# Performance work log

Measured on AMD Instinct MI355X. Metric: run time of the kernel, lower is better.

## Reference

```python
import jax, jax.numpy as jnp
import numpy as np
import math

L, V, D, H, T, B = 12, 50257, 1024, 16, 1024, 1
HD = D // H
EPS = 1e-5


def layernorm(x, g, b):
    m = jnp.mean(x, axis=-1, keepdims=True)
    v = jnp.var(x, axis=-1, keepdims=True)
    return (x - m) * jax.lax.rsqrt(v + EPS) * g + b


def gelu_tanh(x):
    return 0.5 * x * (1.0 + jnp.tanh(math.sqrt(2.0 / math.pi) * (x + 0.044715 * x ** 3)))


def setup_inputs() -> dict:
    key = jax.random.key(0)
    ks = jax.random.split(key, 16)
    s = 0.02
    inp = {
        "x": jax.random.randint(ks[0], (B, T), 0, V),
        "attention_mask": jnp.ones((B, T), jnp.float32),
        "tok_emb": jax.random.normal(ks[1], (V, D), jnp.float32) * s,
        "pos_emb": jax.random.normal(ks[2], (T, D), jnp.float32) * s,
        "ln1_g": jnp.ones((L, D), jnp.float32),
        "ln1_b": jnp.zeros((L, D), jnp.float32),
        "qkv_w": jax.random.normal(ks[3], (L, D, 3 * D), jnp.float32) * s,
        "qkv_b": jnp.zeros((L, 3 * D), jnp.float32),
        "out_w": jax.random.normal(ks[4], (L, D, D), jnp.float32) * s,
        "out_b": jnp.zeros((L, D), jnp.float32),
        "ln2_g": jnp.ones((L, D), jnp.float32),
        "ln2_b": jnp.zeros((L, D), jnp.float32),
        "fc1_w": jax.random.normal(ks[5], (L, D, 4 * D), jnp.float32) * s,
        "fc1_b": jnp.zeros((L, 4 * D), jnp.float32),
        "fc2_w": jax.random.normal(ks[6], (L, 4 * D, D), jnp.float32) * s,
        "fc2_b": jnp.zeros((L, D), jnp.float32),
        "lnf_g": jnp.ones((D,), jnp.float32),
        "lnf_b": jnp.zeros((D,), jnp.float32),
        "lm_w": jax.random.normal(ks[7], (V, D), jnp.float32) * s,
    }
    return inp


def reference(x, attention_mask, tok_emb, pos_emb, ln1_g, ln1_b, qkv_w, qkv_b,
              out_w, out_b, ln2_g, ln2_b, fc1_w, fc1_b, fc2_w, fc2_b,
              lnf_g, lnf_b, lm_w):
    Bx, Tx = x.shape
    h = tok_emb[x] + pos_emb[:Tx]  # (B,T,D)
    causal = jnp.tril(jnp.ones((Tx, Tx), bool))  # (T,T)
    amask_add = (1.0 - attention_mask)[:, None, None, :] * jnp.finfo(h.dtype).min
    scale = 1.0 / math.sqrt(HD)

    def block(h, p):
        l1g, l1b, qw, qb, ow, ob, l2g, l2b, f1w, f1b, f2w, f2b = p
        xn = layernorm(h, l1g, l1b)
        qkv = xn @ qw + qb  # (B,T,3D)
        q, k, v = jnp.split(qkv, 3, axis=-1)
        q = q.reshape(Bx, Tx, H, HD).transpose(0, 2, 1, 3)  # (B,H,T,hd)
        k = k.reshape(Bx, Tx, H, HD).transpose(0, 2, 1, 3)
        v = v.reshape(Bx, Tx, H, HD).transpose(0, 2, 1, 3)
        att = jnp.einsum('bhqd,bhkd->bhqk', q, k) * scale
        att = jnp.where(causal, att, -jnp.inf)
        att = att + amask_add
        att = jax.nn.softmax(att, axis=-1)
        wv = jnp.einsum('bhqk,bhkd->bhqd', att, v)
        wv = wv.transpose(0, 2, 1, 3).reshape(Bx, Tx, D)
        h = h + (wv @ ow + ob)
        xn2 = layernorm(h, l2g, l2b)
        ff = gelu_tanh(xn2 @ f1w + f1b) @ f2w + f2b
        return h + ff, None

    params = (ln1_g, ln1_b, qkv_w, qkv_b, out_w, out_b,
              ln2_g, ln2_b, fc1_w, fc1_b, fc2_w, fc2_b)
    h, _ = jax.lax.scan(block, h, params)
    h = layernorm(h, lnf_g, lnf_b)
    logits = jnp.einsum('btd,vd->btv', h, lm_w)
    return logits
```

## Files before the change

kernel.cpp:

```cpp
#include <hip/hip_runtime.h>
#include <hip/hip_bf16.h>
#include <math.h>

#define Lnum 12
#define Tn 1024
#define Dm 1024
#define Hn 16
#define HDn 64
#define Vn 50257

typedef __bf16 bf16;
typedef __bf16 bf16x4 __attribute__((ext_vector_type(4)));
typedef __bf16 bf16x8 __attribute__((ext_vector_type(8)));
typedef float f32x4 __attribute__((ext_vector_type(4)));

__device__ __forceinline__ void gload_lds16(const void* g, void* l) {
    __builtin_amdgcn_global_load_lds(
        (const __attribute__((address_space(1))) void*)g,
        (__attribute__((address_space(3))) void*)l, 16, 0, 0);
}

__device__ __forceinline__ float gelu_f(float x) {
    const float c = 0.7978845608028654f;
    return 0.5f * x * (1.0f + tanhf(c * (x + 0.044715f * x * x * x)));
}

__global__ __launch_bounds__(256) void embed_k(const int* __restrict__ x,
                                               const float* __restrict__ tok,
                                               const float* __restrict__ pos,
                                               float* __restrict__ h) {
    int t = blockIdx.x;
    int id = x[t];
    const float4* tr = (const float4*)(tok + (size_t)id * Dm);
    const float4* pr = (const float4*)(pos + (size_t)t * Dm);
    float4* hr = (float4*)(h + (size_t)t * Dm);
    int i = threadIdx.x;
    float4 a = tr[i], b = pr[i];
    hr[i] = make_float4(a.x + b.x, a.y + b.y, a.z + b.z, a.w + b.w);
}

__device__ __forceinline__ void ln_body(const float* __restrict__ x,
                                        const float* __restrict__ g,
                                        const float* __restrict__ b,
                                        bf16* __restrict__ y, int row,
                                        float* rs, float* rs2) {
    int tid = threadIdx.x;
    const float* xr = x + (size_t)row * Dm;
    float4 v = ((const float4*)xr)[tid];
    float s = v.x + v.y + v.z + v.w;
    float s2 = v.x * v.x + v.y * v.y + v.z * v.z + v.w * v.w;
    rs[tid] = s; rs2[tid] = s2;
    __syncthreads();
    for (int off = 128; off; off >>= 1) {
        if (tid < off) { rs[tid] += rs[tid + off]; rs2[tid] += rs2[tid + off]; }
        __syncthreads();
    }
    float mean = rs[0] * (1.0f / Dm);
    float var = rs2[0] * (1.0f / Dm) - mean * mean;
    float inv = rsqrtf(var + 1e-5f);
    float4 gg = ((const float4*)g)[tid];
    float4 bb = ((const float4*)b)[tid];
    bf16x4 pk;
    pk[0] = (bf16)((v.x - mean) * inv * gg.x + bb.x);
    pk[1] = (bf16)((v.y - mean) * inv * gg.y + bb.y);
    pk[2] = (bf16)((v.z - mean) * inv * gg.z + bb.z);
    pk[3] = (bf16)((v.w - mean) * inv * gg.w + bb.w);
    *(bf16x4*)(y + (size_t)row * Dm + tid * 4) = pk;
}

__device__ __forceinline__ void tconv_body(const float* __restrict__ W,
                                           bf16* __restrict__ WT,
                                           int K, int N, int n0, int k0,
                                           float (*t)[65]) {
    const int tid = threadIdx.x;
    {
        int ty = tid >> 4;
        int tx = tid & 15;
#pragma unroll
        for (int r = 0; r < 4; ++r) {
            int k = r * 16 + ty;
            float4 v = *(const float4*)&W[(size_t)(k0 + k) * N + n0 + tx * 4];
            t[k][tx * 4 + 0] = v.x; t[k][tx * 4 + 1] = v.y;
            t[k][tx * 4 + 2] = v.z; t[k][tx * 4 + 3] = v.w;
        }
    }
    __syncthreads();
    {
        int nrow = tid >> 2;
        int ks = (tid & 3) * 16;
        bf16x8 p0, p1;
#pragma unroll
        for (int j = 0; j < 8; ++j) p0[j] = (bf16)t[ks + j][nrow];
#pragma unroll
        for (int j = 0; j < 8; ++j) p1[j] = (bf16)t[ks + 8 + j][nrow];
        bf16* dst = WT + (size_t)(n0 + nrow) * K + k0 + ks;
        *(bf16x8*)dst = p0;
        *(bf16x8*)(dst + 8) = p1;
    }
}

__global__ __launch_bounds__(256) void tconv_ln_k(const float* __restrict__ qw,
                                                  const float* __restrict__ ow,
                                                  const float* __restrict__ f1,
                                                  const float* __restrict__ f2,
                                                  bf16* __restrict__ Wl,
                                                  const float* __restrict__ h,
                                                  const float* __restrict__ lg,
                                                  const float* __restrict__ lb,
                                                  bf16* __restrict__ xn) {
    __shared__ float smem[64][65];
    int blk = blockIdx.x;
    if (blk < 3072) {
        const float* W; bf16* WT; int K, N, bi;
        if (blk < 768)       { W = qw; WT = Wl;           K = 1024; N = 3072; bi = blk; }
        else if (blk < 1024) { W = ow; WT = Wl + 3145728; K = 1024; N = 1024; bi = blk - 768; }
        else if (blk < 2048) { W = f1; WT = Wl + 4194304; K = 1024; N = 4096; bi = blk - 1024; }
        else                 { W = f2; WT = Wl + 8388608; K = 4096; N = 1024; bi = blk - 2048; }
        int nx = N >> 6;
        tconv_body(W, WT, K, N, (bi % nx) * 64, (bi / nx) * 64, smem);
    } else {
        ln_body(h, lg, lb, xn, blk - 3072, &smem[0][0], &smem[8][0]);
    }
}

__global__ __launch_bounds__(256) void ln_k(const float* __restrict__ x,
                                            const float* __restrict__ g,
                                            const float* __restrict__ b,
                                            bf16* __restrict__ y) {
    __shared__ float rs[256], rs2[256];
    ln_body(x, g, b, y, blockIdx.x, rs, rs2);
}

__global__ __launch_bounds__(256) void lnf_cvt_k(const float* __restrict__ h,
                                                 const float* __restrict__ lg,
                                                 const float* __restrict__ lb,
                                                 bf16* __restrict__ xn,
                                                 const float* __restrict__ lw,
                                                 bf16* __restrict__ lw_bf, int n8) {
    int blk = blockIdx.x;
    if (blk < 1024) {
        __shared__ float rs[256], rs2[256];
        ln_body(h, lg, lb, xn, blk, rs, rs2);
    } else {
        int tid = threadIdx.x;
        for (int i = (blk - 1024) * 256 + tid; i < n8; i += 2048 * 256) {
            float4 f0 = ((const float4*)lw)[i * 2];
            float4 f1 = ((const float4*)lw)[i * 2 + 1];
            bf16x8 pk;
            pk[0] = (bf16)f0.x; pk[1] = (bf16)f0.y; pk[2] = (bf16)f0.z; pk[3] = (bf16)f0.w;
            pk[4] = (bf16)f1.x; pk[5] = (bf16)f1.y; pk[6] = (bf16)f1.z; pk[7] = (bf16)f1.w;
            *(bf16x8*)(lw_bf + (size_t)i * 8) = pk;
        }
    }
}

template <int BM, int BN, int ACT, bool RESID, bool OUTBF, int BMODE, bool NTAIL>
__global__ __launch_bounds__(256) void mgemm_k(const bf16* __restrict__ A,
                                               const void* __restrict__ Btv,
                                               const float* __restrict__ bias,
                                               const float* __restrict__ resid,
                                               void* __restrict__ Cv,
                                               int N, int K, int nbm, int nbn) {
    constexpr int MI = BM / 32;
    constexpr int NJ = BN / 32;
    __shared__ bf16 As[BM * 64];
    __shared__ bf16 Bs[BN * 64];
    const int tid = threadIdx.x;
    const int lane = tid & 63;
    const int wid = tid >> 6;

    const int bfl = blockIdx.x;
    const int xcd = bfl & 7;
    const int t1 = bfl >> 3;
    const int rr = t1 % nbm;
    const int cg = t1 / nbm;
    const int bm = rr * BM;
    const int bn = (cg * 8 + xcd) * BN;

    const int wr = (wid >> 1) * (BM / 2);
    const int wc = (wid & 1) * (BN / 2);
    const int l15 = lane & 15;
    const int l4 = lane >> 4;

    f32x4 acc[MI][NJ] = {};

    const bf16* aSrc[MI * 2];
#pragma unroll
    for (int u = 0; u < BM / 32; ++u) {
        int ch = u * 256 + tid;
        int row = ch >> 3;
        int cb = (ch & 7) * 16;
        int ksw = (cb ^ ((row & 7) << 4)) >> 1;
        aSrc[u] = A + (size_t)(bm + row) * K + ksw;
    }
    const bf16* bSrc[NJ * 2];
    if (BMODE == 0) {
        const bf16* B = (const bf16*)Btv;
#pragma unroll
        for (int u = 0; u < BN / 32; ++u) {
            int ch = u * 256 + tid;
            int row = ch >> 3;
            int cb = (ch & 7) * 16;
            int ksw = (cb ^ ((row & 7) << 4)) >> 1;
            bSrc[u] = B + (size_t)(bn + row) * K + ksw;
        }
    }

    for (int k0 = 0; k0 < K; k0 += 64) {
#pragma unroll
        for (int u = 0; u < BM / 32; ++u)
            gload_lds16(aSrc[u] + k0, &As[u * 2048 + wid * 512]);
        if (BMODE == 0) {
#pragma unroll
            for (int u = 0; u < BN / 32; ++u)
                gload_lds16(bSrc[u] + k0, &Bs[u * 2048 + wid * 512]);
        } else {
            const float* B = (const float*)Btv;
#pragma unroll
            for (int it = 0; it < BN / 32; ++it) {
                int gi = it * 256 + tid;
                int row = gi >> 3;
                int cb = (gi & 7) * 16;
                int n = bn + row;
                if (NTAIL && n >= N) n = N - 1;
                const float* g = B + (size_t)n * K + k0 + (gi & 7) * 8;
                float4 f0 = *(const float4*)g;
                float4 f1 = *(const float4*)(g + 4);
                bf16x8 pk;
                pk[0] = (bf16)f0.x; pk[1] = (bf16)f0.y; pk[2] = (bf16)f0.z; pk[3] = (bf16)f0.w;
                pk[4] = (bf16)f1.x; pk[5] = (bf16)f1.y; pk[6] = (bf16)f1.z; pk[7] = (bf16)f1.w;
                *(bf16x8*)((char*)Bs + row * 128 + (cb ^ ((row & 7) << 4))) = pk;
            }
        }
        __syncthreads();

#pragma unroll
        for (int kk = 0; kk < 2; ++kk) {
            const int kb = kk * 64 + l4 * 16;
            bf16x8 a[MI], b[NJ];
#pragma unroll
            for (int i = 0; i < MI; ++i) {
                int row = wr + i * 16 + l15;
                a[i] = *(const bf16x8*)((char*)As + row * 128 + (kb ^ ((row & 7) << 4)));
            }
#pragma unroll
            for (int j = 0; j < NJ; ++j) {
                int row = wc + j * 16 + l15;
                b[j] = *(const bf16x8*)((char*)Bs + row * 128 + (kb ^ ((row & 7) << 4)));
            }
#pragma unroll
            for (int i = 0; i < MI; ++i)
#pragma unroll
                for (int j = 0; j < NJ; ++j)
                    acc[i][j] = __builtin_amdgcn_mfma_f32_16x16x32_bf16(a[i], b[j], acc[i][j], 0, 0, 0);
        }
        __syncthreads();
    }

#pragma unroll
    for (int i = 0; i < MI; ++i) {
        int row0 = bm + wr + i * 16 + l4 * 4;
#pragma unroll
        for (int j = 0; j < NJ; ++j) {
            int col = bn + wc + j * 16 + l15;
            if (NTAIL && col >= N) continue;
            float bv = bias ? bias[col] : 0.f;
#pragma unroll
            for (int r = 0; r < 4; ++r) {
                float v = acc[i][j][r] + bv;
                if (ACT == 1) v = gelu_f(v);
                size_t idx = (size_t)(row0 + r) * N + col;
                if (RESID) v += resid[idx];
                if (OUTBF) ((bf16*)Cv)[idx] = (bf16)v;
                else       ((float*)Cv)[idx] = v;
            }
        }
    }
}

__global__ __launch_bounds__(128) void fattn_k(const bf16* __restrict__ qkv,
                                               const float* __restrict__ amask,
                                               bf16* __restrict__ out) {
    __shared__ bf16 Ks[64 * 64];
    __shared__ bf16 Vt[64 * 64];
    __shared__ bf16 Pw[2][16 * 64];
    __shared__ float addb[Tn];
    __shared__ float bcast[2][16];

    const int f = blockIdx.x;
    const int hh = f & 15;
    const int s = f >> 4;
    const int qt = (s < 16) ? s : 47 - s;
    const int tid = threadIdx.x;
    const int lane = tid & 63;
    const int wq = tid >> 6;
    const int l15 = lane & 15;
    const int g = lane >> 4;

    const int qglob = qt * 32 + wq * 16 + l15;
    const int nkt = (qt >> 1) + 1;
    const int kmax = nkt * 64;

    for (int i = tid; i < kmax; i += 128)
        addb[i] = (1.0f - amask[i]) * -3.0e38f;

    bf16x8 qreg[2];
    {
        const bf16* qp = qkv + (size_t)qglob * (3 * Dm) + hh * HDn + g * 8;
        qreg[0] = *(const bf16x8*)qp;
        qreg[1] = *(const bf16x8*)(qp + 32);
    }

    f32x4 accO[4] = {};
    float mrun = -3.0e38f, lrun = 0.f;

    for (int kt = 0; kt < nkt; ++kt) {
        const int kb = kt * 64;
        __syncthreads();
#pragma unroll
        for (int t2 = 0; t2 < 4; ++t2) {
            int c = tid + t2 * 128;
            int kr = c >> 3;
            int d8 = (c & 7) * 8;
            const bf16* gp = qkv + (size_t)(kb + kr) * (3 * Dm) + Dm + hh * HDn + d8;
            bf16x8 v = *(const bf16x8*)gp;
            *(bf16x8*)((char*)Ks + kr * 128 + ((d8 * 2) ^ ((kr & 7) << 4))) = v;
        }
#pragma unroll
        for (int t2 = 0; t2 < 4; ++t2) {
            int c = tid + t2 * 128;
            int k = c >> 3, d0 = (c & 7) * 8;
            const bf16* gp = qkv + (size_t)(kb + k) * (3 * Dm) + 2 * Dm + hh * HDn + d0;
            bf16x8 v = *(const bf16x8*)gp;
#pragma unroll
            for (int j = 0; j < 8; ++j) {
                int d = d0 + j;
                *(bf16*)((char*)Vt + d * 128 + ((2 * k) ^ ((d & 7) << 4))) = v[j];
            }
        }
        __syncthreads();

        f32x4 accS[4] = {};
        __builtin_amdgcn_s_setprio(1);
#pragma unroll
        for (int s2 = 0; s2 < 2; ++s2)
#pragma unroll
            for (int mf = 0; mf < 4; ++mf) {
                int kr = mf * 16 + l15;
                bf16x8 af = *(const bf16x8*)((char*)Ks + kr * 128 + ((s2 * 64 + g * 16) ^ ((kr & 7) << 4)));
                accS[mf] = __builtin_amdgcn_mfma_f32_16x16x32_bf16(af, qreg[s2], accS[mf], 0, 0, 0);
            }
        __builtin_amdgcn_s_setprio(0);

        float p[16];
        float tmax = -3.0e38f;
#pragma unroll
        for (int mf = 0; mf < 4; ++mf)
#pragma unroll
            for (int r = 0; r < 4; ++r) {
                int k = kb + mf * 16 + g * 4 + r;
                float sv = accS[mf][r] * 0.125f + addb[k];
                if (k > qglob) sv = -3.0e38f;
                p[mf * 4 + r] = sv;
                tmax = fmaxf(tmax, sv);
            }
        tmax = fmaxf(tmax, __shfl_xor(tmax, 16, 64));
        tmax = fmaxf(tmax, __shfl_xor(tmax, 32, 64));
        float mnew = fmaxf(mrun, tmax);
        float alpha = expf(mrun - mnew);
        float psum = 0.f;
#pragma unroll
        for (int i = 0; i < 16; ++i) { float e = expf(p[i] - mnew); p[i] = e; psum += e; }
        psum += __shfl_xor(psum, 16, 64);
        psum += __shfl_xor(psum, 32, 64);
        lrun = lrun * alpha + psum;
        mrun = mnew;

        if (g == 0) bcast[wq][l15] = alpha;
        f32x4 av = *(f32x4*)&bcast[wq][g * 4];
#pragma unroll
        for (int nf = 0; nf < 4; ++nf)
#pragma unroll
            for (int r = 0; r < 4; ++r) accO[nf][r] *= av[r];

        char* pw = (char*)Pw[wq];
#pragma unroll
        for (int mf = 0; mf < 4; ++mf) {
            bf16x4 pk;
            pk[0] = (bf16)p[mf * 4 + 0]; pk[1] = (bf16)p[mf * 4 + 1];
            pk[2] = (bf16)p[mf * 4 + 2]; pk[3] = (bf16)p[mf * 4 + 3];
            *(bf16x4*)(pw + l15 * 128 + ((32 * mf + 8 * g) ^ ((l15 & 7) << 4))) = pk;
        }
        bf16x8 pa[2];
#pragma unroll
        for (int s2 = 0; s2 < 2; ++s2)
            pa[s2] = *(const bf16x8*)(pw + l15 * 128 + ((s2 * 64 + g * 16) ^ ((l15 & 7) << 4)));

        __builtin_amdgcn_s_setprio(1);
#pragma unroll
        for (int s2 = 0; s2 < 2; ++s2)
#pragma unroll
            for (int nf = 0; nf < 4; ++nf) {
                int d = nf * 16 + l15;
                bf16x8 bfg = *(const bf16x8*)((char*)Vt + d * 128 + ((s2 * 64 + g * 16) ^ ((d & 7) << 4)));
                accO[nf] = __builtin_amdgcn_mfma_f32_16x16x32_bf16(pa[s2], bfg, accO[nf], 0, 0, 0);
            }
        __builtin_amdgcn_s_setprio(0);
    }

    if (g == 0) bcast[wq][l15] = 1.0f / lrun;
    f32x4 lv = *(f32x4*)&bcast[wq][g * 4];
#pragma unroll
    for (int nf = 0; nf < 4; ++nf)
#pragma unroll
        for (int r = 0; r < 4; ++r) {
            int row = qt * 32 + wq * 16 + 4 * g + r;
            int col = hh * HDn + nf * 16 + l15;
            out[(size_t)row * Dm + col] = (bf16)(accO[nf][r] * lv[r]);
        }
}

extern "C" void kernel_launch(void* const* d_in, const int* in_sizes, int n_in,
                              void* d_out, int out_size, void* d_ws, size_t ws_size,
                              hipStream_t stream) {
    const int*   x      = (const int*)d_in[0];
    const float* amask  = (const float*)d_in[1];
    const float* tok    = (const float*)d_in[2];
    const float* pos    = (const float*)d_in[3];
    const float* ln1_g  = (const float*)d_in[4];
    const float* ln1_b  = (const float*)d_in[5];
    const float* qkv_w  = (const float*)d_in[6];
    const float* qkv_b  = (const float*)d_in[7];
    const float* out_w  = (const float*)d_in[8];
    const float* out_b  = (const float*)d_in[9];
    const float* ln2_g  = (const float*)d_in[10];
    const float* ln2_b  = (const float*)d_in[11];
    const float* fc1_w  = (const float*)d_in[12];
    const float* fc1_b  = (const float*)d_in[13];
    const float* fc2_w  = (const float*)d_in[14];
    const float* fc2_b  = (const float*)d_in[15];
    const float* lnf_g  = (const float*)d_in[16];
    const float* lnf_b  = (const float*)d_in[17];
    const float* lm_w   = (const float*)d_in[18];

    char* ws = (char*)d_ws;
    float* h      = (float*)(ws + 0);
    bf16*  qkv_bf = (bf16*) (ws + (4u << 20));
    bf16*  xn_bf  = (bf16*) (ws + (16u << 20));
    bf16*  wv_bf  = (bf16*) (ws + (18u << 20));
    bf16*  ff1_bf = (bf16*) (ws + (20u << 20));
    bf16*  Wbuf   = (bf16*) (ws + (28u << 20));
    bf16* qT  = Wbuf;
    bf16* oT  = qT  + 3145728;
    bf16* f1T = oT  + 1048576;
    bf16* f2T = f1T + 4194304;
    bf16* lm_bf = (bf16*)(ws + (52u << 20));
    float* outf = (float*)d_out;

    const bool big_ws = ws_size >= ((size_t)153 << 20);

    embed_k<<<Tn, 256, 0, stream>>>(x, tok, pos, h);

    for (int l = 0; l < Lnum; ++l) {
        const float* l1g = ln1_g + (size_t)l * Dm;
        const float* l1b = ln1_b + (size_t)l * Dm;
        const float* qw  = qkv_w + (size_t)l * Dm * 3 * Dm;
        const float* qb  = qkv_b + (size_t)l * 3 * Dm;
        const float* ow  = out_w + (size_t)l * Dm * Dm;
        const float* ob  = out_b + (size_t)l * Dm;
        const float* l2g = ln2_g + (size_t)l * Dm;
        const float* l2b = ln2_b + (size_t)l * Dm;
        const float* f1w = fc1_w + (size_t)l * Dm * 4 * Dm;
        const float* f1b = fc1_b + (size_t)l * 4 * Dm;
        const float* f2w = fc2_w + (size_t)l * 4 * Dm * Dm;
        const float* f2b = fc2_b + (size_t)l * Dm;

        tconv_ln_k<<<4096, 256, 0, stream>>>(qw, ow, f1w, f2w, Wbuf, h, l1g, l1b, xn_bf);
        mgemm_k<64, 64, 0, false, true, 0, false><<<768, 256, 0, stream>>>(
            xn_bf, qT, qb, nullptr, qkv_bf, 3 * Dm, Dm, 16, 48);
        fattn_k<<<512, 128, 0, stream>>>(qkv_bf, amask, wv_bf);
        mgemm_k<32, 64, 0, true, false, 0, false><<<512, 256, 0, stream>>>(
            wv_bf, oT, ob, h, h, Dm, Dm, 32, 16);
        ln_k<<<Tn, 256, 0, stream>>>(h, l2g, l2b, xn_bf);
        mgemm_k<64, 64, 1, false, true, 0, false><<<1024, 256, 0, stream>>>(
            xn_bf, f1T, f1b, nullptr, ff1_bf, 4 * Dm, Dm, 16, 64);
        mgemm_k<32, 64, 0, true, false, 0, false><<<512, 256, 0, stream>>>(
            ff1_bf, f2T, f2b, h, h, Dm, 4 * Dm, 32, 16);
    }

    if (big_ws) {
        lnf_cvt_k<<<3072, 256, 0, stream>>>(h, lnf_g, lnf_b, xn_bf, lm_w, lm_bf,
                                            (Vn * Dm) / 8);
        mgemm_k<128, 128, 0, false, false, 0, true><<<8 * 400, 256, 0, stream>>>(
            xn_bf, lm_bf, nullptr, nullptr, outf, Vn, Dm, 8, 400);
    } else {
        ln_k<<<Tn, 256, 0, stream>>>(h, lnf_g, lnf_b, xn_bf);
        mgemm_k<128, 128, 0, false, false, 1, true><<<8 * 400, 256, 0, stream>>>(
            xn_bf, lm_w, nullptr, nullptr, outf, Vn, Dm, 8, 400);
    }
}
```

Baseline: 1.819 ms.

## Double-buffer LDS in LM-head GEMM and widen FC1 tile to 64x128

Result: slower. 1.892 ms (+4.0%).

```diff
diff --git a/kernel.cpp b/kernel.cpp
--- a/kernel.cpp
+++ b/kernel.cpp
@@ -18,6 +18,11 @@
     __builtin_amdgcn_global_load_lds(
         (const __attribute__((address_space(1))) void*)g,
         (__attribute__((address_space(3))) void*)l, 16, 0, 0);
+}
+
+template <int N> __device__ __forceinline__ void vm_wait() {
+    if constexpr (N == 0)      asm volatile("s_waitcnt vmcnt(0)" ::: "memory");
+    else if constexpr (N == 8) asm volatile("s_waitcnt vmcnt(8)" ::: "memory");
 }
 
 __device__ __forceinline__ float gelu_f(float x) {
@@ -154,7 +159,7 @@
     }
 }
 
-template <int BM, int BN, int ACT, bool RESID, bool OUTBF, int BMODE, bool NTAIL>
+template <int BM, int BN, int ACT, bool RESID, bool OUTBF, int BMODE, bool NTAIL, bool DBUF>
 __global__ __launch_bounds__(256) void mgemm_k(const bf16* __restrict__ A,
                                                const void* __restrict__ Btv,
                                                const float* __restrict__ bias,
@@ -163,8 +168,9 @@
                                                int N, int K, int nbm, int nbn) {
     constexpr int MI = BM / 32;
     constexpr int NJ = BN / 32;
-    __shared__ bf16 As[BM * 64];
-    __shared__ bf16 Bs[BN * 64];
+    constexpr int NBUF = DBUF ? 2 : 1;
+    __shared__ bf16 As[NBUF * BM * 64];
+    __shared__ bf16 Bs[NBUF * BN * 64];
     const int tid = threadIdx.x;
     const int lane = tid & 63;
     const int wid = tid >> 6;
@@ -206,34 +212,18 @@
         }
     }
 
-    for (int k0 = 0; k0 < K; k0 += 64) {
+    auto stage = [&](int half, int k0) {
 #pragma unroll
         for (int u = 0; u < BM / 32; ++u)
-            gload_lds16(aSrc[u] + k0, &As[u * 2048 + wid * 512]);
-        if (BMODE == 0) {
-#pragma unroll
-            for (int u = 0; u < BN / 32; ++u)
-                gload_lds16(bSrc[u] + k0, &Bs[u * 2048 + wid * 512]);
-        } else {
-            const float* B = (const float*)Btv;
-#pragma unroll
-            for (int it = 0; it < BN / 32; ++it) {
-                int gi = it * 256 + tid;
-                int row = gi >> 3;
-                int cb = (gi & 7) * 16;
-                int n = bn + row;
-                if (NTAIL && n >= N) n = N - 1;
-                const float* g = B + (size_t)n * K + k0 + (gi & 7) * 8;
-                float4 f0 = *(const float4*)g;
-                float4 f1 = *(const float4*)(g + 4);
-                bf16x8 pk;
-                pk[0] = (bf16)f0.x; pk[1] = (bf16)f0.y; pk[2] = (bf16)f0.z; pk[3] = (bf16)f0.w;
-                pk[4] = (bf16)f1.x; pk[5] = (bf16)f1.y; pk[6] = (bf16)f1.z; pk[7] = (bf16)f1.w;
-                *(bf16x8*)((char*)Bs + row * 128 + (cb ^ ((row & 7) << 4))) = pk;
-            }
-        }
-        __syncthreads();
-
+            gload_lds16(aSrc[u] + k0, &As[half * BM * 64 + u * 2048 + wid * 512]);
+#pragma unroll
+        for (int u = 0; u < BN / 32; ++u)
+            gload_lds16(bSrc[u] + k0, &Bs[half * BN * 64 + u * 2048 + wid * 512]);
+    };
+
+    auto compute = [&](int half) {
+        const char* aB = (const char*)&As[half * BM * 64];
+        const char* bB = (const char*)&Bs[half * BN * 64];
 #pragma unroll
         for (int kk = 0; kk < 2; ++kk) {
             const int kb = kk * 64 + l4 * 16;
@@ -241,12 +231,12 @@
 #pragma unroll
             for (int i = 0; i < MI; ++i) {
                 int row = wr + i * 16 + l15;
-                a[i] = *(const bf16x8*)((char*)As + row * 128 + (kb ^ ((row & 7) << 4)));
+                a[i] = *(const bf16x8*)(aB + row * 128 + (kb ^ ((row & 7) << 4)));
             }
 #pragma unroll
             for (int j = 0; j < NJ; ++j) {
                 int row = wc + j * 16 + l15;
-                b[j] = *(const bf16x8*)((char*)Bs + row * 128 + (kb ^ ((row & 7) << 4)));
+                b[j] = *(const bf16x8*)(bB + row * 128 + (kb ^ ((row & 7) << 4)));
             }
 #pragma unroll
             for (int i = 0; i < MI; ++i)
@@ -254,7 +244,54 @@
                 for (int j = 0; j < NJ; ++j)
                     acc[i][j] = __builtin_amdgcn_mfma_f32_16x16x32_bf16(a[i], b[j], acc[i][j], 0, 0, 0);
         }
-        __syncthreads();
+    };
+
+    if constexpr (DBUF) {
+        static_assert(BMODE == 0, "DBUF requires bf16 B");
+        const int nt = K >> 6;
+        stage(0, 0);
+        int cur = 0;
+        for (int t = 0; t < nt; ++t) {
+            if (t + 1 < nt) {
+                stage(cur ^ 1, (t + 1) << 6);
+                vm_wait<8>();
+            } else {
+                vm_wait<0>();
+            }
+            asm volatile("s_barrier" ::: "memory");
+            compute(cur);
+            asm volatile("s_barrier" ::: "memory");
+            cur ^= 1;
+        }
+    } else {
+        for (int k0 = 0; k0 < K; k0 += 64) {
+            if (BMODE == 0) {
+                stage(0, k0);
+            } else {
+                const float* B = (const float*)Btv;
+#pragma unroll
+                for (int u = 0; u < BM / 32; ++u)
+                    gload_lds16(aSrc[u] + k0, &As[u * 2048 + wid * 512]);
+#pragma unroll
+                for (int it = 0; it < BN / 32; ++it) {
+                    int gi = it * 256 + tid;
+                    int row = gi >> 3;
+                    int cb = (gi & 7) * 16;
+                    int n = bn + row;
+                    if (NTAIL && n >= N) n = N - 1;
+                    const float* g = B + (size_t)n * K + k0 + (gi & 7) * 8;
+                    float4 f0 = *(const float4*)g;
+                    float4 f1 = *(const float4*)(g + 4);
+                    bf16x8 pk;
+                    pk[0] = (bf16)f0.x; pk[1] = (bf16)f0.y; pk[2] = (bf16)f0.z; pk[3] = (bf16)f0.w;
+                    pk[4] = (bf16)f1.x; pk[5] = (bf16)f1.y; pk[6] = (bf16)f1.z; pk[7] = (bf16)f1.w;
+                    *(bf16x8*)((char*)Bs + row * 128 + (cb ^ ((row & 7) << 4))) = pk;
+                }
+            }
+            __syncthreads();
+            compute(0);
+            __syncthreads();
+        }
     }
 
 #pragma unroll
@@ -476,26 +513,26 @@
         const float* f2b = fc2_b + (size_t)l * Dm;
 
         tconv_ln_k<<<4096, 256, 0, stream>>>(qw, ow, f1w, f2w, Wbuf, h, l1g, l1b, xn_bf);
-        mgemm_k<64, 64, 0, false, true, 0, false><<<768, 256, 0, stream>>>(
+        mgemm_k<64, 64, 0, false, true, 0, false, false><<<768, 256, 0, stream>>>(
             xn_bf, qT, qb, nullptr, qkv_bf, 3 * Dm, Dm, 16, 48);
         fattn_k<<<512, 128, 0, stream>>>(qkv_bf, amask, wv_bf);
-        mgemm_k<32, 64, 0, true, false, 0, false><<<512, 256, 0, stream>>>(
+        mgemm_k<32, 64, 0, true, false, 0, false, false><<<512, 256, 0, stream>>>(
             wv_bf, oT, ob, h, h, Dm, Dm, 32, 16);
         ln_k<<<Tn, 256, 0, stream>>>(h, l2g, l2b, xn_bf);
-        mgemm_k<64, 64, 1, false, true, 0, false><<<1024, 256, 0, stream>>>(
-            xn_bf, f1T, f1b, nullptr, ff1_bf, 4 * Dm, Dm, 16, 64);
-        mgemm_k<32, 64, 0, true, false, 0, false><<<512, 256, 0, stream>>>(
+        mgemm_k<64, 128, 1, false, true, 0, false, false><<<512, 256, 0, stream>>>(
+            xn_bf, f1T, f1b, nullptr, ff1_bf, 4 * Dm, Dm, 16, 32);
+        mgemm_k<32, 64, 0, true, false, 0, false, false><<<512, 256, 0, stream>>>(
             ff1_bf, f2T, f2b, h, h, Dm, 4 * Dm, 32, 16);
     }
 
     if (big_ws) {
         lnf_cvt_k<<<3072, 256, 0, stream>>>(h, lnf_g, lnf_b, xn_bf, lm_w, lm_bf,
                                             (Vn * Dm) / 8);
-        mgemm_k<128, 128, 0, false, false, 0, true><<<8 * 400, 256, 0, stream>>>(
+        mgemm_k<128, 128, 0, false, false, 0, true, true><<<8 * 400, 256, 0, stream>>>(
             xn_bf, lm_bf, nullptr, nullptr, outf, Vn, Dm, 8, 400);
     } else {
         ln_k<<<Tn, 256, 0, stream>>>(h, lnf_g, lnf_b, xn_bf);
-        mgemm_k<128, 128, 0, false, false, 1, true><<<8 * 400, 256, 0, stream>>>(
+        mgemm_k<128, 128, 0, false, false, 1, true, false><<<8 * 400, 256, 0, stream>>>(
             xn_bf, lm_w, nullptr, nullptr, outf, Vn, Dm, 8, 400);
     }
 }
```
